# Performance work log

Measured on AMD Instinct MI355X. Metric: run time of the kernel, lower is better.

The kernel has to match this reference:

```python
import jax, jax.numpy as jnp
import numpy as np

N, D_IN, D_OUT = 8192, 1024, 1024


def setup_inputs() -> dict:
    key = jax.random.key(0)
    k_x, k_q, k_k, k_v = jax.random.split(key, 4)
    scale = 1.0 / np.sqrt(D_IN)
    return {
        "X": jax.random.normal(k_x, (N, D_IN), dtype=jnp.float32),
        "W_q": jax.random.normal(k_q, (D_IN, D_OUT), dtype=jnp.float32) * scale,
        "W_k": jax.random.normal(k_k, (D_IN, D_OUT), dtype=jnp.float32) * scale,
        "W_v": jax.random.normal(k_v, (D_IN, D_OUT), dtype=jnp.float32) * scale,
    }


def reference(X, W_q, W_k, W_v):
    # Projections: [N, d_in] @ [d_in, d_out] -> [N, d_out]
    Q = X @ W_q
    K = X @ W_k
    V = X @ W_v
    d_k = K.shape[-1]
    # Full N x N attention scores (naive, unfused as in the original)
    scores = (Q @ K.T) / jnp.sqrt(jnp.asarray(d_k, dtype=Q.dtype))
    attn = jax.nn.softmax(scores, axis=-1)
    context = attn @ V  # [N, d_out]
    return context
```

## Files before the change

kernel.cpp:

```cpp
#include <hip/hip_runtime.h>
#include <stdint.h>

typedef _Float16 f16;
typedef _Float16 half8 __attribute__((ext_vector_type(8)));
typedef _Float16 half4v __attribute__((ext_vector_type(4)));
typedef float f32x4 __attribute__((ext_vector_type(4)));

#define MB (1024ull * 1024ull)
#define WT_OFF 0ull
#define QH_OFF (6ull * MB)
#define KH_OFF (22ull * MB)
#define VT_OFF (38ull * MB)
#define PH_OFF (54ull * MB)
#define LP2_OFF (182ull * MB)
#define LI_OFF (186ull * MB)

__device__ __forceinline__ half8 cvt8(float4 a, float4 b) {
  half8 h;
  h[0] = (f16)a.x; h[1] = (f16)a.y; h[2] = (f16)a.z; h[3] = (f16)a.w;
  h[4] = (f16)b.x; h[5] = (f16)b.y; h[6] = (f16)b.z; h[7] = (f16)b.w;
  return h;
}

__device__ __forceinline__ void gload16(const void* g, uint32_t lds_off) {
  __builtin_amdgcn_global_load_lds(
      (__attribute__((address_space(1))) void*)(uintptr_t)g,
      (__attribute__((address_space(3))) void*)lds_off, 16, 0, 0);
}

__global__ void k_wt(const float* __restrict__ Wq, const float* __restrict__ Wk,
                     const float* __restrict__ Wv, f16* __restrict__ Wt) {
  __shared__ float tile[32][33];
  const int z = blockIdx.z;
  const float* W = (z == 0) ? Wq : ((z == 1) ? Wk : Wv);
  f16* dst = Wt + z * (1024 * 1024);
  const int tx = threadIdx.x, ty = threadIdx.y;
  const int r0 = blockIdx.y * 32, c0 = blockIdx.x * 32;
#pragma unroll
  for (int i = 0; i < 32; i += 8)
    tile[ty + i][tx] = W[(r0 + ty + i) * 1024 + c0 + tx];
  __syncthreads();
#pragma unroll
  for (int i = 0; i < 32; i += 8)
    dst[(c0 + ty + i) * 1024 + r0 + tx] = (f16)tile[tx][ty + i];
}

__launch_bounds__(256, 2)
__global__ void k_proj(const float* __restrict__ X, const f16* __restrict__ Wt,
                       f16* __restrict__ Qh, f16* __restrict__ Kh, f16* __restrict__ Vt) {
  __shared__ f16 As[2][128][40];
  __shared__ f16 Bs[2][128][40];
  const int z = blockIdx.z;
  const f16* Wz = Wt + z * (1024 * 1024);
  const int m0 = blockIdx.x * 128, n0 = blockIdx.y * 128;
  const int t = threadIdx.x;
  const int w = t >> 6, l = t & 63;
  const int wr = w >> 1, wc = w & 1;
  const int lr = l & 15, lk = (l >> 4) * 8;
  const int sr = t >> 1, sh = t & 1;

  const float* xsrc = X + (m0 + sr) * 1024 + sh * 16;
  const f16*   bsrc = Wz + (n0 + sr) * 1024 + sh * 16;

  f32x4 acc[4][4] = {};

  {
    float4 v0 = *(const float4*)(xsrc + 0);
    float4 v1 = *(const float4*)(xsrc + 4);
    float4 v2 = *(const float4*)(xsrc + 8);
    float4 v3 = *(const float4*)(xsrc + 12);
    *(half8*)(&As[0][sr][sh * 16 + 0]) = cvt8(v0, v1);
    *(half8*)(&As[0][sr][sh * 16 + 8]) = cvt8(v2, v3);
    *(half8*)(&Bs[0][sr][sh * 16 + 0]) = *(const half8*)(bsrc + 0);
    *(half8*)(&Bs[0][sr][sh * 16 + 8]) = *(const half8*)(bsrc + 8);
  }
  __syncthreads();

#pragma unroll 1
  for (int kt = 0; kt < 32; ++kt) {
    const int cur = kt & 1;
    float4 v0, v1, v2, v3;
    half8 b0, b1;
    if (kt < 31) {
      const float* xs = xsrc + (kt + 1) * 32;
      v0 = *(const float4*)(xs + 0);
      v1 = *(const float4*)(xs + 4);
      v2 = *(const float4*)(xs + 8);
      v3 = *(const float4*)(xs + 12);
      const f16* bs = bsrc + (kt + 1) * 32;
      b0 = *(const half8*)(bs + 0);
      b1 = *(const half8*)(bs + 8);
    }
    half8 af[4], bf[4];
#pragma unroll
    for (int mi = 0; mi < 4; ++mi)
      af[mi] = *(const half8*)(&As[cur][wr * 64 + mi * 16 + lr][lk]);
#pragma unroll
    for (int ni = 0; ni < 4; ++ni)
      bf[ni] = *(const half8*)(&Bs[cur][wc * 64 + ni * 16 + lr][lk]);
#pragma unroll
    for (int mi = 0; mi < 4; ++mi)
#pragma unroll
      for (int ni = 0; ni < 4; ++ni)
        acc[mi][ni] = __builtin_amdgcn_mfma_f32_16x16x32_f16(af[mi], bf[ni], acc[mi][ni], 0, 0, 0);
    if (kt < 31) {
      *(half8*)(&As[cur ^ 1][sr][sh * 16 + 0]) = cvt8(v0, v1);
      *(half8*)(&As[cur ^ 1][sr][sh * 16 + 8]) = cvt8(v2, v3);
      *(half8*)(&Bs[cur ^ 1][sr][sh * 16 + 0]) = b0;
      *(half8*)(&Bs[cur ^ 1][sr][sh * 16 + 8]) = b1;
    }
    __syncthreads();
  }

  if (z < 2) {
    f16* dst = (z == 0) ? Qh : Kh;
#pragma unroll
    for (int mi = 0; mi < 4; ++mi)
#pragma unroll
      for (int ni = 0; ni < 4; ++ni) {
        const int row = m0 + wr * 64 + mi * 16 + (l >> 4) * 4;
        const int col = n0 + wc * 64 + ni * 16 + lr;
#pragma unroll
        for (int r = 0; r < 4; ++r)
          dst[(row + r) * 1024 + col] = (f16)acc[mi][ni][r];
      }
  } else {
#pragma unroll
    for (int mi = 0; mi < 4; ++mi)
#pragma unroll
      for (int ni = 0; ni < 4; ++ni) {
        const int row = m0 + wr * 64 + mi * 16 + (l >> 4) * 4;
        const int col = n0 + wc * 64 + ni * 16 + lr;
        half4v v = {(f16)acc[mi][ni][0], (f16)acc[mi][ni][1],
                    (f16)acc[mi][ni][2], (f16)acc[mi][ni][3]};
        *(half4v*)(&Vt[col * 8192 + row]) = v;
      }
  }
}

template <int WN, int BN, int NK, int LDA, int LDB, bool PVE>
__launch_bounds__(512, 2)
__global__ void k_g8(const f16* __restrict__ Ag, const f16* __restrict__ Bg,
                     f16* __restrict__ Pg, float* __restrict__ lpart,
                     const float* __restrict__ linv, float* __restrict__ outp) {
  constexpr int WM = 8 / WN;
  constexpr int WTM = 256 / WM;
  constexpr int NRM = WTM / 16;
  constexpr int BKS = BN * 64;
  constexpr int NLB = BN / 128;
  constexpr int BBASE = 65536;
  constexpr int VM = 2 * (2 + NLB);
  constexpr int NTN = (PVE ? 1024 : 8192) / BN;
  constexpr int CPX = (32 * NTN) / 8;

  __shared__ __align__(128) char smem[BBASE + 4 * BKS];

  const int t = threadIdx.x;
  const int w = t >> 6, l = t & 63;
  const int lr = l & 15, g = l >> 4;
  const int wr = w / WN, wc = w % WN;
  const int bid = blockIdx.x;
  const int swz = (bid & 7) * CPX + (bid >> 3);
  const int mt = swz / NTN, ntl = swz % NTN;
  const int m0 = mt * 256, n0 = ntl * BN;

  const uint32_t lds0 = (uint32_t)(uintptr_t)(void*)smem;
  const int lq = l >> 2, ls = l & 3;
  const int sw = (ls ^ ((lq >> 1) & 3)) << 3;
  const int rdsw = (g ^ ((lr >> 1) & 3)) << 4;

  auto stA = [&](int kS, int ks, int b) {
#pragma unroll
    for (int j = 0; j < 2; ++j) {
      const int rl = w * 32 + j * 16 + lq;
      gload16(Ag + (size_t)(m0 + rl) * LDA + kS * 64 + ks * 32 + sw,
              lds0 + b * 32768 + ks * 16384 + (w * 2 + j) * 1024);
    }
  };
  auto stB = [&](int kS, int ks, int b) {
#pragma unroll
    for (int j = 0; j < NLB; ++j) {
      const int rl = w * (16 * NLB) + j * 16 + lq;
      gload16(Bg + (size_t)(n0 + rl) * LDB + kS * 64 + ks * 32 + sw,
              lds0 + BBASE + b * (2 * BKS) + ks * BKS + (w * NLB + j) * 1024);
    }
  };

  f32x4 acc[NRM][4] = {};

  stA(0, 0, 0); stB(0, 0, 0);
  stA(0, 1, 0); stB(0, 1, 0);
  stA(1, 0, 1); stB(1, 0, 1);
  asm volatile("s_waitcnt vmcnt(%0)" :: "i"(VM));
  __builtin_amdgcn_s_barrier();

#pragma unroll 1
  for (int kt = 0; kt < NK; ++kt) {
    const int b = kt & 1;
    const int k1 = (kt + 1 < NK) ? kt + 1 : kt;
    const int k2 = (kt + 2 < NK) ? kt + 2 : kt;
#pragma unroll
    for (int ks = 0; ks < 2; ++ks) {
      half8 af[NRM], bf[4];
#pragma unroll
      for (int mi = 0; mi < NRM; ++mi)
        af[mi] = *(const half8*)(smem + b * 32768 + ks * 16384 +
                                 (wr * WTM + mi * 16 + lr) * 64 + rdsw);
#pragma unroll
      for (int ni = 0; ni < 4; ++ni)
        bf[ni] = *(const half8*)(smem + BBASE + b * (2 * BKS) + ks * BKS +
                                 (wc * 64 + ni * 16 + lr) * 64 + rdsw);
      if (ks == 0) { stA(k1, 1, b ^ 1); stB(k1, 1, b ^ 1); }
      else         { stA(k2, 0, b);     stB(k2, 0, b); }
      asm volatile("s_waitcnt vmcnt(%0)" :: "i"(VM));
      __builtin_amdgcn_s_barrier();
      __builtin_amdgcn_s_setprio(1);
#pragma unroll
      for (int mi = 0; mi < NRM; ++mi)
#pragma unroll
        for (int ni = 0; ni < 4; ++ni)
          acc[mi][ni] = __builtin_amdgcn_mfma_f32_16x16x32_f16(af[mi], bf[ni], acc[mi][ni], 0, 0, 0);
      __builtin_amdgcn_s_setprio(0);
      __builtin_amdgcn_s_barrier();
    }
  }
  asm volatile("s_waitcnt vmcnt(0)");
  __builtin_amdgcn_s_barrier();

  if constexpr (!PVE) {
    float rs[NRM][4];
#pragma unroll
    for (int mi = 0; mi < NRM; ++mi)
#pragma unroll
      for (int r = 0; r < 4; ++r) rs[mi][r] = 0.f;
#pragma unroll
    for (int mi = 0; mi < NRM; ++mi)
#pragma unroll
      for (int ni = 0; ni < 4; ++ni)
#pragma unroll
        for (int r = 0; r < 4; ++r) {
          const float p = exp2f(acc[mi][ni][r] * 0.045084222f);
          acc[mi][ni][r] = p;
          rs[mi][r] += p;
        }
#pragma unroll
    for (int mi = 0; mi < NRM; ++mi)
#pragma unroll
      for (int r = 0; r < 4; ++r) {
        float v = rs[mi][r];
        v += __shfl_xor(v, 1); v += __shfl_xor(v, 2);
        v += __shfl_xor(v, 4); v += __shfl_xor(v, 8);
        rs[mi][r] = v;
      }
    if (lr == 0) {
#pragma unroll
      for (int mi = 0; mi < NRM; ++mi)
#pragma unroll
        for (int r = 0; r < 4; ++r)
          lpart[(size_t)(ntl * WN + wc) * 8192 + m0 + wr * WTM + mi * 16 + g * 4 + r] = rs[mi][r];
    }
#pragma unroll
    for (int mi = 0; mi < NRM; ++mi)
#pragma unroll
      for (int ni = 0; ni < 4; ++ni)
#pragma unroll
        for (int r = 0; r < 4; ++r)
          *(f16*)(smem + (wr * WTM + mi * 16 + g * 4 + r) * 512 +
                  (wc * 64 + ni * 16 + lr) * 2) = (f16)acc[mi][ni][r];
    __syncthreads();
    {
      const int row = t >> 1, sl = t & 1;
#pragma unroll
      for (int q = 0; q < 16; ++q)
        *(int4*)(Pg + (size_t)(m0 + row) * 8192 + n0 + sl * 128 + q * 8) =
            *(const int4*)(smem + row * 512 + sl * 256 + q * 16);
    }
  } else {
#pragma unroll
    for (int mi = 0; mi < NRM; ++mi) {
#pragma unroll
      for (int r = 0; r < 4; ++r) {
        const int rowg = m0 + wr * WTM + mi * 16 + g * 4 + r;
        const float iv = linv[rowg];
#pragma unroll
        for (int ni = 0; ni < 4; ++ni)
          outp[(size_t)rowg * 1024 + n0 + wc * 64 + ni * 16 + lr] = acc[mi][ni][r] * iv;
      }
    }
  }
}

__global__ void k_lred(const float* __restrict__ lpart, float* __restrict__ linv) {
  const int r = blockIdx.x * 256 + threadIdx.x;
  float s = 0.f;
#pragma unroll
  for (int i = 0; i < 128; ++i) s += lpart[(size_t)i * 8192 + r];
  linv[r] = 1.0f / s;
}

extern "C" void kernel_launch(void* const* d_in, const int* in_sizes, int n_in,
                              void* d_out, int out_size, void* d_ws, size_t ws_size,
                              hipStream_t stream) {
  (void)in_sizes; (void)n_in; (void)out_size; (void)ws_size;
  const float* X  = (const float*)d_in[0];
  const float* Wq = (const float*)d_in[1];
  const float* Wk = (const float*)d_in[2];
  const float* Wv = (const float*)d_in[3];
  char* ws = (char*)d_ws;
  f16* Wt = (f16*)(ws + WT_OFF);
  f16* Qh = (f16*)(ws + QH_OFF);
  f16* Kh = (f16*)(ws + KH_OFF);
  f16* Vt = (f16*)(ws + VT_OFF);
  f16* Ph = (f16*)(ws + PH_OFF);
  float* lpart = (float*)(ws + LP2_OFF);
  float* linv  = (float*)(ws + LI_OFF);
  float* out = (float*)d_out;

  k_wt  <<<dim3(32, 32, 3), dim3(32, 8), 0, stream>>>(Wq, Wk, Wv, Wt);
  k_proj<<<dim3(64, 8, 3),  dim3(256),   0, stream>>>(X, Wt, Qh, Kh, Vt);
  k_g8<4, 256, 16, 1024, 1024, false><<<dim3(1024), dim3(512), 0, stream>>>(
      Qh, Kh, Ph, lpart, nullptr, nullptr);
  k_lred<<<dim3(32), dim3(256), 0, stream>>>(lpart, linv);
  k_g8<2, 128, 128, 8192, 8192, true><<<dim3(256), dim3(512), 0, stream>>>(
      Ph, Vt, nullptr, nullptr, linv, out);
}
```

Measured before the change: 456.8 us.

## Add dedicated QK^T softmax-numerator kernel with interleaved prefetch and staged stores

Replaces the generic templated GEMM for the Q·K^T score stage with a specialized 256x256-tile kernel. Global-to-LDS loads for the next K-slices are interleaved between MFMA bursts, with setprio and barriers around each burst. The P tile is staged through LDS so it can be written to global memory as coalesced 16-byte rows. The added barriers and hand-tuned vmcnt waits carry a risk of stalls or ordering mistakes. The exp step uses no max subtraction, relying on the input scale.

```diff
diff --git a/kernel.cpp b/kernel.cpp
--- a/kernel.cpp
+++ b/kernel.cpp
@@ -136,6 +136,167 @@
         *(half4v*)(&Vt[col * 8192 + row]) = v;
       }
   }
+}
+
+__launch_bounds__(512, 2)
+__global__ void k_s4(const f16* __restrict__ Qh, const f16* __restrict__ Kh,
+                     f16* __restrict__ Ph, float* __restrict__ lpart) {
+  constexpr int BBASE = 65536;
+  __shared__ __align__(128) char smem[131072];
+  const int t = threadIdx.x;
+  const int w = t >> 6, l = t & 63;
+  const int lr = l & 15, g = l >> 4;
+  const int wr = w >> 2, wc = w & 3;
+  const int bid = blockIdx.x;
+  const int swz = (bid & 7) * 128 + (bid >> 3);
+  const int mt = swz >> 5, ntl = swz & 31;
+  const int m0 = mt << 8, n0 = ntl << 8;
+
+  const uint32_t lds0 = (uint32_t)(uintptr_t)(void*)smem;
+  const int lq = l >> 2, ls = l & 3;
+  const int sw = (ls ^ ((lq >> 1) & 3)) << 3;
+  const int rdsw = (g ^ ((lr >> 1) & 3)) << 4;
+
+  auto stA = [&](int kS, int ks, int b) {
+#pragma unroll
+    for (int j = 0; j < 2; ++j) {
+      const int rl = w * 32 + j * 16 + lq;
+      gload16(Qh + (size_t)(m0 + rl) * 1024 + kS * 64 + ks * 32 + sw,
+              lds0 + b * 32768 + ks * 16384 + (w * 2 + j) * 1024);
+    }
+  };
+  auto stB = [&](int kS, int ks, int b) {
+#pragma unroll
+    for (int j = 0; j < 2; ++j) {
+      const int rl = w * 32 + j * 16 + lq;
+      gload16(Kh + (size_t)(n0 + rl) * 1024 + kS * 64 + ks * 32 + sw,
+              lds0 + BBASE + b * 32768 + ks * 16384 + (w * 2 + j) * 1024);
+    }
+  };
+
+  f32x4 acc[8][4] = {};
+
+  auto rdA = [&](int b, int ks, int mh, half8* af) {
+#pragma unroll
+    for (int mi = 0; mi < 4; ++mi)
+      af[mi] = *(const half8*)(smem + b * 32768 + ks * 16384 +
+                               (wr * 128 + mh * 64 + mi * 16 + lr) * 64 + rdsw);
+  };
+  auto rdB = [&](int b, int ks, half8* bf) {
+#pragma unroll
+    for (int ni = 0; ni < 4; ++ni)
+      bf[ni] = *(const half8*)(smem + BBASE + b * 32768 + ks * 16384 +
+                               (wc * 64 + ni * 16 + lr) * 64 + rdsw);
+  };
+
+#define VMW asm volatile("s_waitcnt vmcnt(10)")
+#define BAR __builtin_amdgcn_s_barrier()
+#define PR1 __builtin_amdgcn_s_setprio(1)
+#define PR0 __builtin_amdgcn_s_setprio(0)
+
+  stA(0, 0, 0); stB(0, 0, 0);
+  stA(0, 1, 0); stB(0, 1, 0);
+  stB(1, 0, 1); stA(1, 0, 1); stB(1, 1, 1);
+  VMW;
+  BAR;
+
+#pragma unroll 1
+  for (int kt = 0; kt < 16; ++kt) {
+    const int b = kt & 1;
+    const int k1 = (kt + 1 < 16) ? kt + 1 : 15;
+    const int k2 = (kt + 2 < 16) ? kt + 2 : 15;
+    half8 af[4], bf[4];
+    rdA(b, 0, 0, af); rdB(b, 0, bf);
+    stA(k1, 1, b ^ 1);
+    VMW; BAR; PR1;
+#pragma unroll
+    for (int mi = 0; mi < 4; ++mi)
+#pragma unroll
+      for (int ni = 0; ni < 4; ++ni)
+        acc[mi][ni] = __builtin_amdgcn_mfma_f32_16x16x32_f16(af[mi], bf[ni], acc[mi][ni], 0, 0, 0);
+    PR0; BAR;
+    rdA(b, 0, 1, af);
+    stB(k2, 0, b);
+    VMW; BAR; PR1;
+#pragma unroll
+    for (int mi = 0; mi < 4; ++mi)
+#pragma unroll
+      for (int ni = 0; ni < 4; ++ni)
+        acc[4 + mi][ni] = __builtin_amdgcn_mfma_f32_16x16x32_f16(af[mi], bf[ni], acc[4 + mi][ni], 0, 0, 0);
+    PR0; BAR;
+    rdA(b, 1, 0, af); rdB(b, 1, bf);
+    stA(k2, 0, b);
+    VMW; BAR; PR1;
+#pragma unroll
+    for (int mi = 0; mi < 4; ++mi)
+#pragma unroll
+      for (int ni = 0; ni < 4; ++ni)
+        acc[mi][ni] = __builtin_amdgcn_mfma_f32_16x16x32_f16(af[mi], bf[ni], acc[mi][ni], 0, 0, 0);
+    PR0; BAR;
+    rdA(b, 1, 1, af);
+    stB(k2, 1, b);
+    VMW; BAR; PR1;
+#pragma unroll
+    for (int mi = 0; mi < 4; ++mi)
+#pragma unroll
+      for (int ni = 0; ni < 4; ++ni)
+        acc[4 + mi][ni] = __builtin_amdgcn_mfma_f32_16x16x32_f16(af[mi], bf[ni], acc[4 + mi][ni], 0, 0, 0);
+    PR0; BAR;
+  }
+  asm volatile("s_waitcnt vmcnt(0)");
+  BAR;
+
+  float rs[8][4];
+#pragma unroll
+  for (int mi = 0; mi < 8; ++mi)
+#pragma unroll
+    for (int r = 0; r < 4; ++r) rs[mi][r] = 0.f;
+#pragma unroll
+  for (int mi = 0; mi < 8; ++mi)
+#pragma unroll
+    for (int ni = 0; ni < 4; ++ni)
+#pragma unroll
+      for (int r = 0; r < 4; ++r) {
+        const float p = exp2f(acc[mi][ni][r] * 0.045084222f);
+        acc[mi][ni][r] = p;
+        rs[mi][r] += p;
+      }
+#pragma unroll
+  for (int mi = 0; mi < 8; ++mi)
+#pragma unroll
+    for (int r = 0; r < 4; ++r) {
+      float v = rs[mi][r];
+      v += __shfl_xor(v, 1); v += __shfl_xor(v, 2);
+      v += __shfl_xor(v, 4); v += __shfl_xor(v, 8);
+      rs[mi][r] = v;
+    }
+  if (lr == 0) {
+#pragma unroll
+    for (int mi = 0; mi < 8; ++mi)
+#pragma unroll
+      for (int r = 0; r < 4; ++r)
+        lpart[(size_t)(ntl * 4 + wc) * 8192 + m0 + wr * 128 + mi * 16 + g * 4 + r] = rs[mi][r];
+  }
+#pragma unroll
+  for (int mi = 0; mi < 8; ++mi)
+#pragma unroll
+    for (int ni = 0; ni < 4; ++ni)
+#pragma unroll
+      for (int r = 0; r < 4; ++r)
+        *(f16*)(smem + (wr * 128 + mi * 16 + g * 4 + r) * 512 +
+                (wc * 64 + ni * 16 + lr) * 2) = (f16)acc[mi][ni][r];
+  __syncthreads();
+  {
+    const int row = t >> 1, sl = t & 1;
+#pragma unroll
+    for (int q = 0; q < 16; ++q)
+      *(int4*)(Ph + (size_t)(m0 + row) * 8192 + n0 + sl * 128 + q * 8) =
+          *(const int4*)(smem + row * 512 + sl * 256 + q * 16);
+  }
+#undef VMW
+#undef BAR
+#undef PR1
+#undef PR0
 }
 
 template <int WN, int BN, int NK, int LDA, int LDB, bool PVE>
@@ -318,8 +479,7 @@
 
   k_wt  <<<dim3(32, 32, 3), dim3(32, 8), 0, stream>>>(Wq, Wk, Wv, Wt);
   k_proj<<<dim3(64, 8, 3),  dim3(256),   0, stream>>>(X, Wt, Qh, Kh, Vt);
-  k_g8<4, 256, 16, 1024, 1024, false><<<dim3(1024), dim3(512), 0, stream>>>(
-      Qh, Kh, Ph, lpart, nullptr, nullptr);
+  k_s4<<<dim3(1024), dim3(512), 0, stream>>>(Qh, Kh, Ph, lpart);
   k_lred<<<dim3(32), dim3(256), 0, stream>>>(lpart, linv);
   k_g8<2, 128, 128, 8192, 8192, true><<<dim3(256), dim3(512), 0, stream>>>(
       Ph, Vt, nullptr, nullptr, linv, out);
```

Result: no change. 456.2 us (-0.1%).

## Split score-exp GEMM into dedicated 128x128-tile kernel and tighten PV scheduling

Applied to the files above, without the earlier changes.

Replaces the templated 256x256-tile Q·K^T/exp path with a dedicated k_sexp kernel. It uses 128x128 tiles, 256 threads, an XOR-swizzled LDS layout and a simple load-sync-compute loop, and writes exp scores plus row partial sums. The PV kernel drops its non-PVE branch and gains sched_barrier fences plus an explicit lgkmcnt wait around its barriers. The aim is higher occupancy and a simpler epilogue for the score GEMM. The trade-off is that the new kernel gives up the double-buffered prefetch pipeline and gets less data reuse per tile.

```diff
diff --git a/kernel.cpp b/kernel.cpp
--- a/kernel.cpp
+++ b/kernel.cpp
@@ -14,6 +14,12 @@
 #define PH_OFF (54ull * MB)
 #define LP2_OFF (182ull * MB)
 #define LI_OFF (186ull * MB)
+
+#define SB __builtin_amdgcn_sched_barrier(0)
+#define BAR __builtin_amdgcn_s_barrier()
+#define PR1 __builtin_amdgcn_s_setprio(1)
+#define PR0 __builtin_amdgcn_s_setprio(0)
+#define LGK0 asm volatile("s_waitcnt lgkmcnt(0)" ::: "memory")
 
 __device__ __forceinline__ half8 cvt8(float4 a, float4 b) {
   half8 h;
@@ -138,10 +144,102 @@
   }
 }
 
-template <int WN, int BN, int NK, int LDA, int LDB, bool PVE>
+__launch_bounds__(256, 2)
+__global__ void k_sexp(const f16* __restrict__ Qh, const f16* __restrict__ Kh,
+                       f16* __restrict__ Ph, float* __restrict__ lpart) {
+  __shared__ __align__(128) char smem[32768];
+  const int t = threadIdx.x;
+  const int w = t >> 6, l = t & 63;
+  const int wr = w >> 1, wc = w & 1;
+  const int lr = l & 15, g = l >> 4;
+  const int bid = blockIdx.x;
+  const int swz = ((bid & 7) << 9) | (bid >> 3);
+  const int mt = swz >> 6, nt = swz & 63;
+  const int m0 = mt << 7, n0 = nt << 7;
+
+  const uint32_t lds0 = (uint32_t)(uintptr_t)(void*)smem;
+  f32x4 acc[4][4] = {};
+
+#pragma unroll 1
+  for (int kt = 0; kt < 16; ++kt) {
+#pragma unroll
+    for (int i = 0; i < 4; ++i) {
+      const int r = ((i << 8) + t) >> 3;
+      const int sl = (t & 7) ^ (r & 7);
+      gload16(Qh + (size_t)(m0 + r) * 1024 + (kt << 6) + (sl << 3),
+              lds0 + (i << 12) + (w << 10));
+      gload16(Kh + (size_t)(n0 + r) * 1024 + (kt << 6) + (sl << 3),
+              lds0 + 16384 + (i << 12) + (w << 10));
+    }
+    __syncthreads();
+#pragma unroll
+    for (int ks = 0; ks < 2; ++ks) {
+      half8 af[4], bf[4];
+#pragma unroll
+      for (int mi = 0; mi < 4; ++mi) {
+        const int row = wr * 64 + mi * 16 + lr;
+        const int sp = ((ks << 2) + g) ^ (row & 7);
+        af[mi] = *(const half8*)(smem + row * 128 + sp * 16);
+      }
+#pragma unroll
+      for (int ni = 0; ni < 4; ++ni) {
+        const int row = wc * 64 + ni * 16 + lr;
+        const int sp = ((ks << 2) + g) ^ (row & 7);
+        bf[ni] = *(const half8*)(smem + 16384 + row * 128 + sp * 16);
+      }
+#pragma unroll
+      for (int mi = 0; mi < 4; ++mi)
+#pragma unroll
+        for (int ni = 0; ni < 4; ++ni)
+          acc[mi][ni] = __builtin_amdgcn_mfma_f32_16x16x32_f16(af[mi], bf[ni], acc[mi][ni], 0, 0, 0);
+    }
+    __syncthreads();
+  }
+
+  float rs[4][4] = {};
+#pragma unroll
+  for (int mi = 0; mi < 4; ++mi)
+#pragma unroll
+    for (int ni = 0; ni < 4; ++ni)
+#pragma unroll
+      for (int r = 0; r < 4; ++r) {
+        const float p = exp2f(acc[mi][ni][r] * 0.045084222f);
+        rs[mi][r] += p;
+        const int row = wr * 64 + mi * 16 + g * 4 + r;
+        const int col = wc * 64 + ni * 16 + lr;
+        *(f16*)(smem + row * 256 + col * 2) = (f16)p;
+      }
+#pragma unroll
+  for (int mi = 0; mi < 4; ++mi)
+#pragma unroll
+    for (int r = 0; r < 4; ++r) {
+      float v = rs[mi][r];
+      v += __shfl_xor(v, 1);
+      v += __shfl_xor(v, 2);
+      v += __shfl_xor(v, 4);
+      v += __shfl_xor(v, 8);
+      rs[mi][r] = v;
+    }
+  if (lr == 0) {
+#pragma unroll
+    for (int mi = 0; mi < 4; ++mi)
+#pragma unroll
+      for (int r = 0; r < 4; ++r)
+        lpart[(size_t)(nt * 2 + wc) * 8192 + m0 + wr * 64 + mi * 16 + g * 4 + r] = rs[mi][r];
+  }
+  __syncthreads();
+#pragma unroll
+  for (int j = 0; j < 8; ++j) {
+    const int row = j * 16 + (t >> 4);
+    const int c16 = t & 15;
+    *(int4*)(Ph + (size_t)(m0 + row) * 8192 + n0 + c16 * 8) =
+        *(const int4*)(smem + row * 256 + c16 * 16);
+  }
+}
+
+template <int WN, int BN, int NK, int LDA, int LDB>
 __launch_bounds__(512, 2)
 __global__ void k_g8(const f16* __restrict__ Ag, const f16* __restrict__ Bg,
-                     f16* __restrict__ Pg, float* __restrict__ lpart,
                      const float* __restrict__ linv, float* __restrict__ outp) {
   constexpr int WM = 8 / WN;
   constexpr int WTM = 256 / WM;
@@ -149,8 +247,7 @@
   constexpr int BKS = BN * 64;
   constexpr int NLB = BN / 128;
   constexpr int BBASE = 65536;
-  constexpr int VM = 2 * (2 + NLB);
-  constexpr int NTN = (PVE ? 1024 : 8192) / BN;
+  constexpr int NTN = 1024 / BN;
   constexpr int CPX = (32 * NTN) / 8;
 
   __shared__ __align__(128) char smem[BBASE + 4 * BKS];
@@ -191,8 +288,9 @@
   stA(0, 0, 0); stB(0, 0, 0);
   stA(0, 1, 0); stB(0, 1, 0);
   stA(1, 0, 1); stB(1, 0, 1);
-  asm volatile("s_waitcnt vmcnt(%0)" :: "i"(VM));
-  __builtin_amdgcn_s_barrier();
+  asm volatile("s_waitcnt vmcnt(6)" ::: "memory");
+  SB;
+  BAR;
 
 #pragma unroll 1
   for (int kt = 0; kt < NK; ++kt) {
@@ -212,80 +310,28 @@
                                  (wc * 64 + ni * 16 + lr) * 64 + rdsw);
       if (ks == 0) { stA(k1, 1, b ^ 1); stB(k1, 1, b ^ 1); }
       else         { stA(k2, 0, b);     stB(k2, 0, b); }
-      asm volatile("s_waitcnt vmcnt(%0)" :: "i"(VM));
-      __builtin_amdgcn_s_barrier();
-      __builtin_amdgcn_s_setprio(1);
+      asm volatile("s_waitcnt vmcnt(6)" ::: "memory");
+      SB; BAR; LGK0; SB; PR1;
 #pragma unroll
       for (int mi = 0; mi < NRM; ++mi)
 #pragma unroll
         for (int ni = 0; ni < 4; ++ni)
           acc[mi][ni] = __builtin_amdgcn_mfma_f32_16x16x32_f16(af[mi], bf[ni], acc[mi][ni], 0, 0, 0);
-      __builtin_amdgcn_s_setprio(0);
-      __builtin_amdgcn_s_barrier();
-    }
-  }
-  asm volatile("s_waitcnt vmcnt(0)");
-  __builtin_amdgcn_s_barrier();
-
-  if constexpr (!PVE) {
-    float rs[NRM][4];
-#pragma unroll
-    for (int mi = 0; mi < NRM; ++mi)
-#pragma unroll
-      for (int r = 0; r < 4; ++r) rs[mi][r] = 0.f;
-#pragma unroll
-    for (int mi = 0; mi < NRM; ++mi)
+      PR0; SB; BAR;
+    }
+  }
+  asm volatile("s_waitcnt vmcnt(0)" ::: "memory");
+  BAR;
+
+#pragma unroll
+  for (int mi = 0; mi < NRM; ++mi) {
+#pragma unroll
+    for (int r = 0; r < 4; ++r) {
+      const int rowg = m0 + wr * WTM + mi * 16 + g * 4 + r;
+      const float iv = linv[rowg];
 #pragma unroll
       for (int ni = 0; ni < 4; ++ni)
-#pragma unroll
-        for (int r = 0; r < 4; ++r) {
-          const float p = exp2f(acc[mi][ni][r] * 0.045084222f);
-          acc[mi][ni][r] = p;
-          rs[mi][r] += p;
-        }
-#pragma unroll
-    for (int mi = 0; mi < NRM; ++mi)
-#pragma unroll
-      for (int r = 0; r < 4; ++r) {
-        float v = rs[mi][r];
-        v += __shfl_xor(v, 1); v += __shfl_xor(v, 2);
-        v += __shfl_xor(v, 4); v += __shfl_xor(v, 8);
-        rs[mi][r] = v;
-      }
-    if (lr == 0) {
-#pragma unroll
-      for (int mi = 0; mi < NRM; ++mi)
-#pragma unroll
-        for (int r = 0; r < 4; ++r)
-          lpart[(size_t)(ntl * WN + wc) * 8192 + m0 + wr * WTM + mi * 16 + g * 4 + r] = rs[mi][r];
-    }
-#pragma unroll
-    for (int mi = 0; mi < NRM; ++mi)
-#pragma unroll
-      for (int ni = 0; ni < 4; ++ni)
-#pragma unroll
-        for (int r = 0; r < 4; ++r)
-          *(f16*)(smem + (wr * WTM + mi * 16 + g * 4 + r) * 512 +
-                  (wc * 64 + ni * 16 + lr) * 2) = (f16)acc[mi][ni][r];
-    __syncthreads();
-    {
-      const int row = t >> 1, sl = t & 1;
-#pragma unroll
-      for (int q = 0; q < 16; ++q)
-        *(int4*)(Pg + (size_t)(m0 + row) * 8192 + n0 + sl * 128 + q * 8) =
-            *(const int4*)(smem + row * 512 + sl * 256 + q * 16);
-    }
-  } else {
-#pragma unroll
-    for (int mi = 0; mi < NRM; ++mi) {
-#pragma unroll
-      for (int r = 0; r < 4; ++r) {
-        const int rowg = m0 + wr * WTM + mi * 16 + g * 4 + r;
-        const float iv = linv[rowg];
-#pragma unroll
-        for (int ni = 0; ni < 4; ++ni)
-          outp[(size_t)rowg * 1024 + n0 + wc * 64 + ni * 16 + lr] = acc[mi][ni][r] * iv;
-      }
+        outp[(size_t)rowg * 1024 + n0 + wc * 64 + ni * 16 + lr] = acc[mi][ni][r] * iv;
     }
   }
 }
@@ -318,9 +364,8 @@
 
   k_wt  <<<dim3(32, 32, 3), dim3(32, 8), 0, stream>>>(Wq, Wk, Wv, Wt);
   k_proj<<<dim3(64, 8, 3),  dim3(256),   0, stream>>>(X, Wt, Qh, Kh, Vt);
-  k_g8<4, 256, 16, 1024, 1024, false><<<dim3(1024), dim3(512), 0, stream>>>(
-      Qh, Kh, Ph, lpart, nullptr, nullptr);
+  k_sexp<<<dim3(4096), dim3(256), 0, stream>>>(Qh, Kh, Ph, lpart);
   k_lred<<<dim3(32), dim3(256), 0, stream>>>(lpart, linv);
-  k_g8<2, 128, 128, 8192, 8192, true><<<dim3(256), dim3(512), 0, stream>>>(
-      Ph, Vt, nullptr, nullptr, linv, out);
-}
+  k_g8<2, 128, 128, 8192, 8192><<<dim3(256), dim3(512), 0, stream>>>(
+      Ph, Vt, linv, out);
+}
```

Result: no change. 449.6 us (-1.6%).
